# Kernel optimization log

Measured on AMD Instinct MI355X. Metric: run time of the kernel, lower is better.

The kernel has to match this reference:

```python
import jax, jax.numpy as jnp
import numpy as np

N_NODES = 100000
N_EDGES = 3200000


def gcn_conv(x, edge_index, W, b, num_nodes):
    # PyG GCNConv: linear transform, add self-loops, symmetric degree norm, scatter-add, bias
    h = x @ W  # [N, out]
    src = jnp.concatenate([edge_index[0], jnp.arange(num_nodes)])  # self-loops
    dst = jnp.concatenate([edge_index[1], jnp.arange(num_nodes)])
    deg = jax.ops.segment_sum(jnp.ones_like(dst, dtype=h.dtype), dst, num_segments=num_nodes)
    dinv = jnp.where(deg > 0, jax.lax.rsqrt(deg), 0.0)
    norm = dinv[src] * dinv[dst]  # [E+N]
    msg = h[src] * norm[:, None]  # gather + scale
    out = jax.ops.segment_sum(msg, dst, num_segments=num_nodes)  # scatter-add
    return out + b


def setup_inputs() -> dict:
    key = jax.random.key(0)
    k1, k2, k3, k4 = jax.random.split(key, 4)
    x = jax.random.normal(k1, (N_NODES, 18), dtype=jnp.float32)
    edge_index = jax.random.randint(k2, (2, N_EDGES), 0, N_NODES, dtype=jnp.int64)
    W1 = jax.random.normal(k3, (18, 64), dtype=jnp.float32) * (1.0 / np.sqrt(18))
    b1 = jnp.zeros((64,), dtype=jnp.float32)
    W2 = jax.random.normal(k4, (64, 32), dtype=jnp.float32) * (1.0 / np.sqrt(64))
    b2 = jnp.zeros((32,), dtype=jnp.float32)
    return {"x": x, "edge_index": edge_index, "W1": W1, "b1": b1, "W2": W2, "b2": b2}


def reference(x, edge_index, W1, b1, W2, b2):
    h = jax.nn.relu(gcn_conv(x, edge_index, W1, b1, N_NODES))
    return gcn_conv(h, edge_index, W2, b2, N_NODES)
```

## Files before the change

kernel.cpp:

```cpp
#include <hip/hip_runtime.h>
#include <hip/hip_fp16.h>

#define F0 18
#define F1 64
#define F2 32
#define BSHIFT 8
#define BNODES 256
#define CHUNK 8192
#define NSTRIPE 8
#define CAPS 1280
#define CAPB (CAPS * NSTRIPE)

__global__ __launch_bounds__(256) void scatter32_kernel(const int* __restrict__ ei,
                                                        int* __restrict__ bcur,
                                                        unsigned int* __restrict__ stage,
                                                        int E, int NB) {
    __shared__ int lh[512];
    __shared__ int lb[512];
    int t = threadIdx.x;
    int s = blockIdx.x & (NSTRIPE - 1);
    for (int i = t; i < NB; i += 256) lh[i] = 0;
    __syncthreads();
    int e0 = blockIdx.x * CHUNK, e1 = min(e0 + CHUNK, E);
    for (int e = e0 + t; e < e1; e += 256)
        atomicAdd(&lh[ei[E + e] >> BSHIFT], 1);
    __syncthreads();
    for (int i = t; i < NB; i += 256) {
        int c = lh[i];
        lb[i] = c ? atomicAdd(&bcur[i * NSTRIPE + s], c) : 0;
        lh[i] = 0;
    }
    __syncthreads();
    for (int e = e0 + t; e < e1; e += 256) {
        int sN = ei[e], d = ei[E + e];
        int b = d >> BSHIFT;
        int off = lb[b] + atomicAdd(&lh[b], 1);
        if (off < CAPS)
            stage[(size_t)(b * NSTRIPE + s) * CAPS + off] =
                ((unsigned)(d & 255) << 24) | (unsigned)sN;
    }
}

__global__ __launch_bounds__(1024) void bucketfill_kernel(const unsigned int* __restrict__ stage,
                                                          const int* __restrict__ bcur,
                                                          int* __restrict__ rps,
                                                          int* __restrict__ rpe,
                                                          float* __restrict__ dinv,
                                                          int* __restrict__ csr,
                                                          const float* __restrict__ x,
                                                          __half* __restrict__ xp, int n) {
    __shared__ unsigned int sbuf[CAPB];
    __shared__ int lcnt[BNODES];
    __shared__ int lofs[BNODES];
    __shared__ float ldv[BNODES];
    __shared__ int segofs[NSTRIPE + 1];
    int b = blockIdx.x;
    int base = b << BSHIFT;
    int nn = min(BNODES, n - base);
    int estart = b * CAPB;
    int t = threadIdx.x;

    if (t == 0) {
        int acc = 0;
        for (int s = 0; s < NSTRIPE; ++s) {
            segofs[s] = acc;
            acc += min(bcur[b * NSTRIPE + s], CAPS);
        }
        segofs[NSTRIPE] = acc;
    }
    if (t < BNODES) lcnt[t] = 0;
    __syncthreads();
    int ecnt = segofs[NSTRIPE];

    for (int s = 0; s < NSTRIPE; ++s) {
        int so = segofs[s], cs = segofs[s + 1] - so;
        const unsigned int* src = stage + (size_t)(b * NSTRIPE + s) * CAPS;
        for (int i = t; i < cs; i += 1024) sbuf[so + i] = src[i];
    }
    __syncthreads();

    for (int e = t; e < ecnt; e += 1024)
        atomicAdd(&lcnt[sbuf[e] >> 24], 1);
    __syncthreads();

    int v = 0;
    if (t < BNODES) { v = (t < nn) ? lcnt[t] : 0; lofs[t] = v; }
    __syncthreads();
    for (int off = 1; off < BNODES; off <<= 1) {
        int xv = 0;
        if (t < BNODES && t >= off) xv = lofs[t - off];
        __syncthreads();
        if (t < BNODES) lofs[t] += xv;
        __syncthreads();
    }
    if (t < nn) {
        float dv = rsqrtf((float)(v + 1));
        rps[base + t] = estart + lofs[t] - v;
        rpe[base + t] = estart + lofs[t];
        dinv[base + t] = dv;
        ldv[t] = dv;
    }
    __syncthreads();
    if (t < BNODES) lcnt[t] = lofs[t] - v;
    __syncthreads();

    for (int e = t; e < ecnt; e += 1024) {
        unsigned int pk = sbuf[e];
        int d = pk >> 24;
        int pos = atomicAdd(&lcnt[d], 1);
        csr[estart + pos] = (int)(pk & 0xffffffu);
    }
    for (int idx = t; idx < nn * 32; idx += 1024) {
        int lv = idx >> 5, j = idx & 31;
        float val = (j < F0) ? ldv[lv] * x[(size_t)(base + lv) * F0 + j] : 0.f;
        xp[(size_t)(base + lv) * 32 + j] = __float2half(val);
    }
}

struct __align__(8) h4v { __half2 a, b; };

__global__ __launch_bounds__(256) void agg32h_kernel(const __half* __restrict__ tab,
                                                     const int* __restrict__ csr,
                                                     const int* __restrict__ rps,
                                                     const int* __restrict__ rpe,
                                                     const float* __restrict__ dinv,
                                                     const float* __restrict__ bias,
                                                     float* __restrict__ outp, int n) {
    int wid = (blockIdx.x * 256 + threadIdx.x) >> 6;
    int lane = threadIdx.x & 63;
    if (wid >= n) return;
    int sub = lane >> 3;
    int q = (lane & 7) << 2;
    int beg = rps[wid], end = rpe[wid];
    float4 acc = make_float4(0.f, 0.f, 0.f, 0.f);
    if (sub == 0) {
        h4v sv = *(const h4v*)&tab[(size_t)wid * 32 + q];
        float2 f0 = __half22float2(sv.a), f1 = __half22float2(sv.b);
        acc.x = f0.x; acc.y = f0.y; acc.z = f1.x; acc.w = f1.y;
    }
    int e = beg + sub;
    for (; e + 8 < end; e += 16) {
        int s0 = csr[e], s1 = csr[e + 8];
        h4v v0 = *(const h4v*)&tab[(size_t)s0 * 32 + q];
        h4v v1 = *(const h4v*)&tab[(size_t)s1 * 32 + q];
        float2 a0 = __half22float2(v0.a), b0 = __half22float2(v0.b);
        float2 a1 = __half22float2(v1.a), b1 = __half22float2(v1.b);
        acc.x += a0.x + a1.x; acc.y += a0.y + a1.y;
        acc.z += b0.x + b1.x; acc.w += b0.y + b1.y;
    }
    for (; e < end; e += 8) {
        int s0 = csr[e];
        h4v v0 = *(const h4v*)&tab[(size_t)s0 * 32 + q];
        float2 a0 = __half22float2(v0.a), b0 = __half22float2(v0.b);
        acc.x += a0.x; acc.y += a0.y; acc.z += b0.x; acc.w += b0.y;
    }
    for (int off = 8; off < 64; off <<= 1) {
        acc.x += __shfl_xor(acc.x, off, 64);
        acc.y += __shfl_xor(acc.y, off, 64);
        acc.z += __shfl_xor(acc.z, off, 64);
        acc.w += __shfl_xor(acc.w, off, 64);
    }
    if (sub == 0) {
        float dv = dinv[wid];
        float4 r;
        r.x = acc.x * dv; r.y = acc.y * dv; r.z = acc.z * dv; r.w = acc.w * dv;
        if (bias) { r.x += bias[q]; r.y += bias[q + 1]; r.z += bias[q + 2]; r.w += bias[q + 3]; }
        *(float4*)&outp[(size_t)wid * 32 + q] = r;
    }
}

__global__ __launch_bounds__(256) void gemm_fused_kernel(const float* __restrict__ ax,
                                                         const float* __restrict__ W1,
                                                         const float* __restrict__ b1,
                                                         const float* __restrict__ W2,
                                                         const float* __restrict__ dinv,
                                                         __half* __restrict__ h2p, int n) {
    __shared__ float W1s[F0 * F1];
    __shared__ float W2s[F1 * F2];
    __shared__ float hid[8][F1];
    __shared__ float axs[8][32];
    int t = threadIdx.x;
    for (int i = t; i < F0 * F1; i += 256) W1s[i] = W1[i];
    for (int i = t; i < F1 * F2; i += 256) W2s[i] = W2[i];
    int lv = t >> 5, j = t & 31;
    int v = blockIdx.x * 8 + lv;
    if (v < n) axs[lv][j] = ax[(size_t)v * 32 + j];
    __syncthreads();
    float h0 = b1[j], h1 = b1[j + 32];
#pragma unroll
    for (int k = 0; k < F0; ++k) {
        float a = axs[lv][k];
        h0 += a * W1s[k * F1 + j];
        h1 += a * W1s[k * F1 + j + 32];
    }
    hid[lv][j] = fmaxf(h0, 0.f);
    hid[lv][j + 32] = fmaxf(h1, 0.f);
    __syncthreads();
    float acc = 0.f;
#pragma unroll
    for (int k = 0; k < F1; ++k) acc += hid[lv][k] * W2s[k * F2 + j];
    if (v < n) h2p[(size_t)v * 32 + j] = __float2half(acc * dinv[v]);
}


extern "C" void kernel_launch(void* const* d_in, const int* in_sizes, int n_in,
                              void* d_out, int out_size, void* d_ws, size_t ws_size,
                              hipStream_t stream) {
    const float* x  = (const float*)d_in[0];
    const int*   ei = (const int*)d_in[1];
    const float* W1 = (const float*)d_in[2];
    const float* b1 = (const float*)d_in[3];
    const float* W2 = (const float*)d_in[4];
    const float* b2 = (const float*)d_in[5];
    float* out = (float*)d_out;

    int n = in_sizes[0] / F0;
    int E = in_sizes[1] / 2;
    int NB = (n + BNODES - 1) >> BSHIFT;

    char* ws = (char*)d_ws;
    size_t o = 0;
    auto alloc = [&](size_t bytes) {
        char* p = ws + o;
        o = (o + bytes + 255) & ~(size_t)255;
        return p;
    };
    int*   rps   = (int*)alloc((size_t)n * 4);
    int*   rpe   = (int*)alloc((size_t)n * 4);
    float* dinv  = (float*)alloc((size_t)n * 4);
    int*   bcur  = (int*)alloc((size_t)NB * NSTRIPE * 4);
    int*   csr   = (int*)alloc((size_t)NB * CAPB * 4);
    unsigned int* stage = (unsigned int*)alloc((size_t)NB * CAPB * 4);
    float* ax    = (float*)alloc((size_t)n * 32 * 4);
    __half* xp   = (__half*)alloc((size_t)n * 32 * 2);
    __half* h2p  = (__half*)stage;
    (void)ws_size; (void)n_in; (void)out_size;

    int nchunks = (E + CHUNK - 1) / CHUNK;

    hipMemsetAsync(bcur, 0, (size_t)NB * NSTRIPE * 4, stream);
    scatter32_kernel<<<nchunks, 256, 0, stream>>>(ei, bcur, stage, E, NB);
    bucketfill_kernel<<<NB, 1024, 0, stream>>>(stage, bcur, rps, rpe, dinv, csr, x, xp, n);

    agg32h_kernel<<<(n + 3) / 4, 256, 0, stream>>>(xp, csr, rps, rpe, dinv, nullptr, ax, n);
    gemm_fused_kernel<<<(n + 7) / 8, 256, 0, stream>>>(ax, W1, b1, W2, dinv, h2p, n);
    agg32h_kernel<<<(n + 3) / 4, 256, 0, stream>>>(h2p, csr, rps, rpe, dinv, b2, out, n);
}
```

Baseline: 217.0 us.

## Split gathered feature tables into narrow 16-column and 2-column half tables

The padded 32-wide half feature table is replaced by column-split tables. For layer 1 that is a 16-column table plus a 2-column table, so the 14 padding columns are no longer gathered. Layer 2 becomes two 16-column halves aggregated in separate passes, which keeps each gathered row at 32 bytes so it fits the cache better. Index loads are marked nontemporal. In exchange there are more kernel launches and the CSR index array is read more times, and the bias pointer arithmetic has to be correct for the split halves.

```diff
diff --git a/kernel.cpp b/kernel.cpp
--- a/kernel.cpp
+++ b/kernel.cpp
@@ -23,7 +23,7 @@
     __syncthreads();
     int e0 = blockIdx.x * CHUNK, e1 = min(e0 + CHUNK, E);
     for (int e = e0 + t; e < e1; e += 256)
-        atomicAdd(&lh[ei[E + e] >> BSHIFT], 1);
+        atomicAdd(&lh[__builtin_nontemporal_load(&ei[E + e]) >> BSHIFT], 1);
     __syncthreads();
     for (int i = t; i < NB; i += 256) {
         int c = lh[i];
@@ -32,7 +32,8 @@
     }
     __syncthreads();
     for (int e = e0 + t; e < e1; e += 256) {
-        int sN = ei[e], d = ei[E + e];
+        int sN = __builtin_nontemporal_load(&ei[e]);
+        int d  = __builtin_nontemporal_load(&ei[E + e]);
         int b = d >> BSHIFT;
         int off = lb[b] + atomicAdd(&lh[b], 1);
         if (off < CAPS)
@@ -48,7 +49,9 @@
                                                           float* __restrict__ dinv,
                                                           int* __restrict__ csr,
                                                           const float* __restrict__ x,
-                                                          __half* __restrict__ xp, int n) {
+                                                          __half* __restrict__ xpA,
+                                                          __half* __restrict__ xpB,
+                                                          int n) {
     __shared__ unsigned int sbuf[CAPB];
     __shared__ int lcnt[BNODES];
     __shared__ int lofs[BNODES];
@@ -110,51 +113,58 @@
         int pos = atomicAdd(&lcnt[d], 1);
         csr[estart + pos] = (int)(pk & 0xffffffu);
     }
-    for (int idx = t; idx < nn * 32; idx += 1024) {
-        int lv = idx >> 5, j = idx & 31;
-        float val = (j < F0) ? ldv[lv] * x[(size_t)(base + lv) * F0 + j] : 0.f;
-        xp[(size_t)(base + lv) * 32 + j] = __float2half(val);
+    for (int idx = t; idx < nn * 16; idx += 1024) {
+        int lv = idx >> 4, j = idx & 15;
+        xpA[(size_t)(base + lv) * 16 + j] =
+            __float2half(ldv[lv] * x[(size_t)(base + lv) * F0 + j]);
+    }
+    for (int idx = t; idx < nn * 2; idx += 1024) {
+        int lv = idx >> 1, j = idx & 1;
+        xpB[(size_t)(base + lv) * 2 + j] =
+            __float2half(ldv[lv] * x[(size_t)(base + lv) * F0 + 16 + j]);
     }
 }
 
 struct __align__(8) h4v { __half2 a, b; };
 
-__global__ __launch_bounds__(256) void agg32h_kernel(const __half* __restrict__ tab,
+__global__ __launch_bounds__(256) void agg16h_kernel(const __half* __restrict__ tab,
                                                      const int* __restrict__ csr,
                                                      const int* __restrict__ rps,
                                                      const int* __restrict__ rpe,
                                                      const float* __restrict__ dinv,
                                                      const float* __restrict__ bias,
-                                                     float* __restrict__ outp, int n) {
+                                                     float* __restrict__ outp,
+                                                     int colofs, int n) {
     int wid = (blockIdx.x * 256 + threadIdx.x) >> 6;
     int lane = threadIdx.x & 63;
     if (wid >= n) return;
-    int sub = lane >> 3;
-    int q = (lane & 7) << 2;
+    int sub = lane >> 2;
+    int q = (lane & 3) << 2;
     int beg = rps[wid], end = rpe[wid];
     float4 acc = make_float4(0.f, 0.f, 0.f, 0.f);
     if (sub == 0) {
-        h4v sv = *(const h4v*)&tab[(size_t)wid * 32 + q];
+        h4v sv = *(const h4v*)&tab[(size_t)wid * 16 + q];
         float2 f0 = __half22float2(sv.a), f1 = __half22float2(sv.b);
         acc.x = f0.x; acc.y = f0.y; acc.z = f1.x; acc.w = f1.y;
     }
     int e = beg + sub;
-    for (; e + 8 < end; e += 16) {
-        int s0 = csr[e], s1 = csr[e + 8];
-        h4v v0 = *(const h4v*)&tab[(size_t)s0 * 32 + q];
-        h4v v1 = *(const h4v*)&tab[(size_t)s1 * 32 + q];
+    for (; e + 16 < end; e += 32) {
+        int s0 = __builtin_nontemporal_load(&csr[e]);
+        int s1 = __builtin_nontemporal_load(&csr[e + 16]);
+        h4v v0 = *(const h4v*)&tab[(size_t)s0 * 16 + q];
+        h4v v1 = *(const h4v*)&tab[(size_t)s1 * 16 + q];
         float2 a0 = __half22float2(v0.a), b0 = __half22float2(v0.b);
         float2 a1 = __half22float2(v1.a), b1 = __half22float2(v1.b);
         acc.x += a0.x + a1.x; acc.y += a0.y + a1.y;
         acc.z += b0.x + b1.x; acc.w += b0.y + b1.y;
     }
-    for (; e < end; e += 8) {
-        int s0 = csr[e];
-        h4v v0 = *(const h4v*)&tab[(size_t)s0 * 32 + q];
+    for (; e < end; e += 16) {
+        int s0 = __builtin_nontemporal_load(&csr[e]);
+        h4v v0 = *(const h4v*)&tab[(size_t)s0 * 16 + q];
         float2 a0 = __half22float2(v0.a), b0 = __half22float2(v0.b);
         acc.x += a0.x; acc.y += a0.y; acc.z += b0.x; acc.w += b0.y;
     }
-    for (int off = 8; off < 64; off <<= 1) {
+    for (int off = 4; off < 64; off <<= 1) {
         acc.x += __shfl_xor(acc.x, off, 64);
         acc.y += __shfl_xor(acc.y, off, 64);
         acc.z += __shfl_xor(acc.z, off, 64);
@@ -165,7 +175,35 @@
         float4 r;
         r.x = acc.x * dv; r.y = acc.y * dv; r.z = acc.z * dv; r.w = acc.w * dv;
         if (bias) { r.x += bias[q]; r.y += bias[q + 1]; r.z += bias[q + 2]; r.w += bias[q + 3]; }
-        *(float4*)&outp[(size_t)wid * 32 + q] = r;
+        *(float4*)&outp[(size_t)wid * 32 + colofs + q] = r;
+    }
+}
+
+__global__ __launch_bounds__(256) void agg2h_kernel(const __half* __restrict__ tab2,
+                                                    const int* __restrict__ csr,
+                                                    const int* __restrict__ rps,
+                                                    const int* __restrict__ rpe,
+                                                    const float* __restrict__ dinv,
+                                                    float* __restrict__ outp, int n) {
+    int wid = (blockIdx.x * 256 + threadIdx.x) >> 6;
+    int lane = threadIdx.x & 63;
+    if (wid >= n) return;
+    int beg = rps[wid], end = rpe[wid];
+    float ax = 0.f, ay = 0.f;
+    for (int e = beg + lane; e < end; e += 64) {
+        int s = __builtin_nontemporal_load(&csr[e]);
+        float2 f = __half22float2(*(const __half2*)&tab2[(size_t)s * 2]);
+        ax += f.x; ay += f.y;
+    }
+    for (int off = 1; off < 64; off <<= 1) {
+        ax += __shfl_xor(ax, off, 64);
+        ay += __shfl_xor(ay, off, 64);
+    }
+    if (lane == 0) {
+        float2 f = __half22float2(*(const __half2*)&tab2[(size_t)wid * 2]);
+        float dv = dinv[wid];
+        outp[(size_t)wid * 32 + 16] = (ax + f.x) * dv;
+        outp[(size_t)wid * 32 + 17] = (ay + f.y) * dv;
     }
 }
 
@@ -174,7 +212,9 @@
                                                          const float* __restrict__ b1,
                                                          const float* __restrict__ W2,
                                                          const float* __restrict__ dinv,
-                                                         __half* __restrict__ h2p, int n) {
+                                                         __half* __restrict__ h2A,
+                                                         __half* __restrict__ h2B,
+                                                         int n) {
     __shared__ float W1s[F0 * F1];
     __shared__ float W2s[F1 * F2];
     __shared__ float hid[8][F1];
@@ -199,7 +239,11 @@
     float acc = 0.f;
 #pragma unroll
     for (int k = 0; k < F1; ++k) acc += hid[lv][k] * W2s[k * F2 + j];
-    if (v < n) h2p[(size_t)v * 32 + j] = __float2half(acc * dinv[v]);
+    if (v < n) {
+        float r = acc * dinv[v];
+        if (j < 16) h2A[(size_t)v * 16 + j] = __float2half(r);
+        else        h2B[(size_t)v * 16 + (j - 16)] = __float2half(r);
+    }
 }
 
 
@@ -232,17 +276,21 @@
     int*   csr   = (int*)alloc((size_t)NB * CAPB * 4);
     unsigned int* stage = (unsigned int*)alloc((size_t)NB * CAPB * 4);
     float* ax    = (float*)alloc((size_t)n * 32 * 4);
-    __half* xp   = (__half*)alloc((size_t)n * 32 * 2);
-    __half* h2p  = (__half*)stage;
+    __half* xpA  = (__half*)alloc((size_t)n * 16 * 2);
+    __half* xpB  = (__half*)alloc((size_t)n * 2 * 2);
+    __half* h2A  = (__half*)stage;
+    __half* h2B  = (__half*)(stage + (size_t)n * 16);
     (void)ws_size; (void)n_in; (void)out_size;
 
     int nchunks = (E + CHUNK - 1) / CHUNK;
 
     hipMemsetAsync(bcur, 0, (size_t)NB * NSTRIPE * 4, stream);
     scatter32_kernel<<<nchunks, 256, 0, stream>>>(ei, bcur, stage, E, NB);
-    bucketfill_kernel<<<NB, 1024, 0, stream>>>(stage, bcur, rps, rpe, dinv, csr, x, xp, n);
-
-    agg32h_kernel<<<(n + 3) / 4, 256, 0, stream>>>(xp, csr, rps, rpe, dinv, nullptr, ax, n);
-    gemm_fused_kernel<<<(n + 7) / 8, 256, 0, stream>>>(ax, W1, b1, W2, dinv, h2p, n);
-    agg32h_kernel<<<(n + 3) / 4, 256, 0, stream>>>(h2p, csr, rps, rpe, dinv, b2, out, n);
-}
+    bucketfill_kernel<<<NB, 1024, 0, stream>>>(stage, bcur, rps, rpe, dinv, csr, x, xpA, xpB, n);
+
+    agg16h_kernel<<<(n + 3) / 4, 256, 0, stream>>>(xpA, csr, rps, rpe, dinv, nullptr, ax, 0, n);
+    agg2h_kernel<<<(n + 3) / 4, 256, 0, stream>>>(xpB, csr, rps, rpe, dinv, ax, n);
+    gemm_fused_kernel<<<(n + 7) / 8, 256, 0, stream>>>(ax, W1, b1, W2, dinv, h2A, h2B, n);
+    agg16h_kernel<<<(n + 3) / 4, 256, 0, stream>>>(h2A, csr, rps, rpe, dinv, b2, out, 0, n);
+    agg16h_kernel<<<(n + 3) / 4, 256, 0, stream>>>(h2B, csr, rps, rpe, dinv, b2 + 16, out, 16, n);
+}
```

Measured after the change: 294.6 us. +35.8%, slower.

## Split aggregation into two source-range phases for gather cache locality

Applied to the files above, without the earlier changes.

Each CSR row is partitioned by whether the source index falls in the lower or upper half of the nodes, and each aggregation runs as two passes, each gathering only from one half of the feature table. The goal is to shrink the gather working set per pass so it fits better in cache. The cost is an extra fp32 partial buffer written and re-read, two more launches, and a 512-bin scan in bucketfill. The scatter kernel also moves to 1024 threads with nontemporal edge loads.

```diff
diff --git a/kernel.cpp b/kernel.cpp
--- a/kernel.cpp
+++ b/kernel.cpp
@@ -11,28 +11,29 @@
 #define CAPS 1280
 #define CAPB (CAPS * NSTRIPE)
 
-__global__ __launch_bounds__(256) void scatter32_kernel(const int* __restrict__ ei,
-                                                        int* __restrict__ bcur,
-                                                        unsigned int* __restrict__ stage,
-                                                        int E, int NB) {
+__global__ __launch_bounds__(1024) void scatter32_kernel(const int* __restrict__ ei,
+                                                         int* __restrict__ bcur,
+                                                         unsigned int* __restrict__ stage,
+                                                         int E, int NB) {
     __shared__ int lh[512];
     __shared__ int lb[512];
     int t = threadIdx.x;
     int s = blockIdx.x & (NSTRIPE - 1);
-    for (int i = t; i < NB; i += 256) lh[i] = 0;
+    if (t < 512) lh[t] = 0;
     __syncthreads();
     int e0 = blockIdx.x * CHUNK, e1 = min(e0 + CHUNK, E);
-    for (int e = e0 + t; e < e1; e += 256)
-        atomicAdd(&lh[ei[E + e] >> BSHIFT], 1);
-    __syncthreads();
-    for (int i = t; i < NB; i += 256) {
+    for (int e = e0 + t; e < e1; e += 1024)
+        atomicAdd(&lh[__builtin_nontemporal_load(&ei[E + e]) >> BSHIFT], 1);
+    __syncthreads();
+    for (int i = t; i < NB; i += 1024) {
         int c = lh[i];
         lb[i] = c ? atomicAdd(&bcur[i * NSTRIPE + s], c) : 0;
         lh[i] = 0;
     }
     __syncthreads();
-    for (int e = e0 + t; e < e1; e += 256) {
-        int sN = ei[e], d = ei[E + e];
+    for (int e = e0 + t; e < e1; e += 1024) {
+        int sN = __builtin_nontemporal_load(&ei[e]);
+        int d  = __builtin_nontemporal_load(&ei[E + e]);
         int b = d >> BSHIFT;
         int off = lb[b] + atomicAdd(&lh[b], 1);
         if (off < CAPS)
@@ -44,14 +45,16 @@
 __global__ __launch_bounds__(1024) void bucketfill_kernel(const unsigned int* __restrict__ stage,
                                                           const int* __restrict__ bcur,
                                                           int* __restrict__ rps,
+                                                          int* __restrict__ mid,
                                                           int* __restrict__ rpe,
                                                           float* __restrict__ dinv,
                                                           int* __restrict__ csr,
                                                           const float* __restrict__ x,
-                                                          __half* __restrict__ xp, int n) {
+                                                          __half* __restrict__ xp,
+                                                          int halfN, int n) {
     __shared__ unsigned int sbuf[CAPB];
-    __shared__ int lcnt[BNODES];
-    __shared__ int lofs[BNODES];
+    __shared__ int lcnt2[512];
+    __shared__ int lofs2[512];
     __shared__ float ldv[BNODES];
     __shared__ int segofs[NSTRIPE + 1];
     int b = blockIdx.x;
@@ -68,7 +71,7 @@
         }
         segofs[NSTRIPE] = acc;
     }
-    if (t < BNODES) lcnt[t] = 0;
+    if (t < 512) lcnt2[t] = 0;
     __syncthreads();
     int ecnt = segofs[NSTRIPE];
 
@@ -79,36 +82,46 @@
     }
     __syncthreads();
 
-    for (int e = t; e < ecnt; e += 1024)
-        atomicAdd(&lcnt[sbuf[e] >> 24], 1);
-    __syncthreads();
-
-    int v = 0;
-    if (t < BNODES) { v = (t < nn) ? lcnt[t] : 0; lofs[t] = v; }
-    __syncthreads();
-    for (int off = 1; off < BNODES; off <<= 1) {
+    for (int e = t; e < ecnt; e += 1024) {
+        unsigned int pk = sbuf[e];
+        int idx = (int)((pk >> 24) << 1) | ((int)(pk & 0xffffffu) >= halfN ? 1 : 0);
+        atomicAdd(&lcnt2[idx], 1);
+    }
+    __syncthreads();
+
+    if (t < 512) lofs2[t] = lcnt2[t];
+    __syncthreads();
+    for (int off = 1; off < 512; off <<= 1) {
         int xv = 0;
-        if (t < BNODES && t >= off) xv = lofs[t - off];
+        if (t < 512 && t >= off) xv = lofs2[t - off];
         __syncthreads();
-        if (t < BNODES) lofs[t] += xv;
+        if (t < 512) lofs2[t] += xv;
         __syncthreads();
     }
     if (t < nn) {
-        float dv = rsqrtf((float)(v + 1));
-        rps[base + t] = estart + lofs[t] - v;
-        rpe[base + t] = estart + lofs[t];
+        int cA = lcnt2[2 * t], cB = lcnt2[2 * t + 1];
+        int incl = lofs2[2 * t + 1];
+        int eB = incl - cB, eA = eB - cA;
+        float dv = rsqrtf((float)(cA + cB + 1));
+        rps[base + t] = estart + eA;
+        mid[base + t] = estart + eB;
+        rpe[base + t] = estart + incl;
         dinv[base + t] = dv;
         ldv[t] = dv;
     }
     __syncthreads();
-    if (t < BNODES) lcnt[t] = lofs[t] - v;
+    int cur = 0;
+    if (t < 512) cur = lofs2[t] - lcnt2[t];
+    __syncthreads();
+    if (t < 512) lcnt2[t] = cur;
     __syncthreads();
 
     for (int e = t; e < ecnt; e += 1024) {
         unsigned int pk = sbuf[e];
-        int d = pk >> 24;
-        int pos = atomicAdd(&lcnt[d], 1);
-        csr[estart + pos] = (int)(pk & 0xffffffu);
+        int src = (int)(pk & 0xffffffu);
+        int idx = (int)((pk >> 24) << 1) | (src >= halfN ? 1 : 0);
+        int pos = atomicAdd(&lcnt2[idx], 1);
+        csr[estart + pos] = src;
     }
     for (int idx = t; idx < nn * 32; idx += 1024) {
         int lv = idx >> 5, j = idx & 31;
@@ -119,21 +132,24 @@
 
 struct __align__(8) h4v { __half2 a, b; };
 
-__global__ __launch_bounds__(256) void agg32h_kernel(const __half* __restrict__ tab,
-                                                     const int* __restrict__ csr,
-                                                     const int* __restrict__ rps,
-                                                     const int* __restrict__ rpe,
-                                                     const float* __restrict__ dinv,
-                                                     const float* __restrict__ bias,
-                                                     float* __restrict__ outp, int n) {
+__global__ __launch_bounds__(256) void aggph_kernel(const __half* __restrict__ tab,
+                                                    const int* __restrict__ csr,
+                                                    const int* __restrict__ begA,
+                                                    const int* __restrict__ endA,
+                                                    const float* __restrict__ dinv,
+                                                    const float* __restrict__ bias,
+                                                    const float* __restrict__ part,
+                                                    float* __restrict__ outp,
+                                                    int phase, int halfN, int n) {
     int wid = (blockIdx.x * 256 + threadIdx.x) >> 6;
     int lane = threadIdx.x & 63;
     if (wid >= n) return;
     int sub = lane >> 3;
     int q = (lane & 7) << 2;
-    int beg = rps[wid], end = rpe[wid];
+    int beg = begA[wid], end = endA[wid];
     float4 acc = make_float4(0.f, 0.f, 0.f, 0.f);
-    if (sub == 0) {
+    bool selfHere = (phase == 0) ? (wid < halfN) : (wid >= halfN);
+    if (sub == 0 && selfHere) {
         h4v sv = *(const h4v*)&tab[(size_t)wid * 32 + q];
         float2 f0 = __half22float2(sv.a), f1 = __half22float2(sv.b);
         acc.x = f0.x; acc.y = f0.y; acc.z = f1.x; acc.w = f1.y;
@@ -161,10 +177,16 @@
         acc.w += __shfl_xor(acc.w, off, 64);
     }
     if (sub == 0) {
-        float dv = dinv[wid];
         float4 r;
-        r.x = acc.x * dv; r.y = acc.y * dv; r.z = acc.z * dv; r.w = acc.w * dv;
-        if (bias) { r.x += bias[q]; r.y += bias[q + 1]; r.z += bias[q + 2]; r.w += bias[q + 3]; }
+        if (phase == 0) {
+            r = acc;
+        } else {
+            const float4 p = *(const float4*)&part[(size_t)wid * 32 + q];
+            float dv = dinv[wid];
+            r.x = (acc.x + p.x) * dv; r.y = (acc.y + p.y) * dv;
+            r.z = (acc.z + p.z) * dv; r.w = (acc.w + p.w) * dv;
+            if (bias) { r.x += bias[q]; r.y += bias[q + 1]; r.z += bias[q + 2]; r.w += bias[q + 3]; }
+        }
         *(float4*)&outp[(size_t)wid * 32 + q] = r;
     }
 }
@@ -217,6 +239,7 @@
     int n = in_sizes[0] / F0;
     int E = in_sizes[1] / 2;
     int NB = (n + BNODES - 1) >> BSHIFT;
+    int halfN = n / 2;
 
     char* ws = (char*)d_ws;
     size_t o = 0;
@@ -226,6 +249,7 @@
         return p;
     };
     int*   rps   = (int*)alloc((size_t)n * 4);
+    int*   midp  = (int*)alloc((size_t)n * 4);
     int*   rpe   = (int*)alloc((size_t)n * 4);
     float* dinv  = (float*)alloc((size_t)n * 4);
     int*   bcur  = (int*)alloc((size_t)NB * NSTRIPE * 4);
@@ -233,16 +257,20 @@
     unsigned int* stage = (unsigned int*)alloc((size_t)NB * CAPB * 4);
     float* ax    = (float*)alloc((size_t)n * 32 * 4);
     __half* xp   = (__half*)alloc((size_t)n * 32 * 2);
-    __half* h2p  = (__half*)stage;
+    __half* h2p  = (__half*)alloc((size_t)n * 32 * 2);
+    float* part  = (float*)stage;
     (void)ws_size; (void)n_in; (void)out_size;
 
     int nchunks = (E + CHUNK - 1) / CHUNK;
 
     hipMemsetAsync(bcur, 0, (size_t)NB * NSTRIPE * 4, stream);
-    scatter32_kernel<<<nchunks, 256, 0, stream>>>(ei, bcur, stage, E, NB);
-    bucketfill_kernel<<<NB, 1024, 0, stream>>>(stage, bcur, rps, rpe, dinv, csr, x, xp, n);
-
-    agg32h_kernel<<<(n + 3) / 4, 256, 0, stream>>>(xp, csr, rps, rpe, dinv, nullptr, ax, n);
+    scatter32_kernel<<<nchunks, 1024, 0, stream>>>(ei, bcur, stage, E, NB);
+    bucketfill_kernel<<<NB, 1024, 0, stream>>>(stage, bcur, rps, midp, rpe, dinv, csr, x, xp, halfN, n);
+
+    int aggblocks = (n + 3) / 4;
+    aggph_kernel<<<aggblocks, 256, 0, stream>>>(xp, csr, rps, midp, dinv, nullptr, nullptr, part, 0, halfN, n);
+    aggph_kernel<<<aggblocks, 256, 0, stream>>>(xp, csr, midp, rpe, dinv, nullptr, part, ax, 1, halfN, n);
     gemm_fused_kernel<<<(n + 7) / 8, 256, 0, stream>>>(ax, W1, b1, W2, dinv, h2p, n);
-    agg32h_kernel<<<(n + 3) / 4, 256, 0, stream>>>(h2p, csr, rps, rpe, dinv, b2, out, n);
-}
+    aggph_kernel<<<aggblocks, 256, 0, stream>>>(h2p, csr, rps, midp, dinv, nullptr, nullptr, part, 0, halfN, n);
+    aggph_kernel<<<aggblocks, 256, 0, stream>>>(h2p, csr, midp, rpe, dinv, b2, part, out, 1, halfN, n);
+}
```

Result: slower. 257.5 us (+18.7%).

## Fuse first-layer aggregation with MLP and widen scatter blocks

Applied to the files above, without the earlier changes.

Merges the first neighbour aggregation with the dense W1/ReLU/W2 transform in one kernel. Each wavefront aggregates one node, stages the result in LDS and runs both matrix products in place, so the fp32 intermediate buffer and its global write and read disappear, along with one launch. The scatter kernel moves to 1024-thread blocks with nontemporal loads of the edge list. The trade-off is that every 4-node block now reloads 16KB of weights into LDS, which adds L2 traffic and LDS pressure.

```diff
diff --git a/kernel.cpp b/kernel.cpp
--- a/kernel.cpp
+++ b/kernel.cpp
@@ -11,28 +11,29 @@
 #define CAPS 1280
 #define CAPB (CAPS * NSTRIPE)
 
-__global__ __launch_bounds__(256) void scatter32_kernel(const int* __restrict__ ei,
-                                                        int* __restrict__ bcur,
-                                                        unsigned int* __restrict__ stage,
-                                                        int E, int NB) {
+__global__ __launch_bounds__(1024) void scatter32_kernel(const int* __restrict__ ei,
+                                                         int* __restrict__ bcur,
+                                                         unsigned int* __restrict__ stage,
+                                                         int E, int NB) {
     __shared__ int lh[512];
     __shared__ int lb[512];
     int t = threadIdx.x;
     int s = blockIdx.x & (NSTRIPE - 1);
-    for (int i = t; i < NB; i += 256) lh[i] = 0;
+    if (t < 512) lh[t] = 0;
     __syncthreads();
     int e0 = blockIdx.x * CHUNK, e1 = min(e0 + CHUNK, E);
-    for (int e = e0 + t; e < e1; e += 256)
-        atomicAdd(&lh[ei[E + e] >> BSHIFT], 1);
-    __syncthreads();
-    for (int i = t; i < NB; i += 256) {
+    for (int e = e0 + t; e < e1; e += 1024)
+        atomicAdd(&lh[__builtin_nontemporal_load(&ei[E + e]) >> BSHIFT], 1);
+    __syncthreads();
+    for (int i = t; i < NB; i += 1024) {
         int c = lh[i];
         lb[i] = c ? atomicAdd(&bcur[i * NSTRIPE + s], c) : 0;
         lh[i] = 0;
     }
     __syncthreads();
-    for (int e = e0 + t; e < e1; e += 256) {
-        int sN = ei[e], d = ei[E + e];
+    for (int e = e0 + t; e < e1; e += 1024) {
+        int sN = __builtin_nontemporal_load(&ei[e]);
+        int d  = __builtin_nontemporal_load(&ei[E + e]);
         int b = d >> BSHIFT;
         int off = lb[b] + atomicAdd(&lh[b], 1);
         if (off < CAPS)
@@ -119,6 +120,82 @@
 
 struct __align__(8) h4v { __half2 a, b; };
 
+__global__ __launch_bounds__(256) void agg1_mlp_kernel(const __half* __restrict__ tab,
+                                                       const int* __restrict__ csr,
+                                                       const int* __restrict__ rps,
+                                                       const int* __restrict__ rpe,
+                                                       const float* __restrict__ dinv,
+                                                       const float* __restrict__ W1,
+                                                       const float* __restrict__ b1,
+                                                       const float* __restrict__ W2,
+                                                       __half* __restrict__ h2p, int n) {
+    __shared__ float W1s[32 * F1];
+    __shared__ float W2s[F1 * F2];
+    __shared__ float ax_lds[4][32];
+    __shared__ float hid_lds[4][F1];
+    int t = threadIdx.x;
+    for (int i = t; i < 32 * F1; i += 256) {
+        int k = i >> 6;
+        W1s[i] = (k < F0) ? W1[(size_t)k * F1 + (i & 63)] : 0.f;
+    }
+    for (int i = t; i < F1 * F2; i += 256) W2s[i] = W2[i];
+    __syncthreads();
+
+    int wid = (blockIdx.x * 256 + t) >> 6;
+    int lane = t & 63;
+    int slot = (t >> 6) & 3;
+    if (wid >= n) return;
+    int sub = lane >> 3;
+    int q = (lane & 7) << 2;
+    int beg = rps[wid], end = rpe[wid];
+    float4 acc = make_float4(0.f, 0.f, 0.f, 0.f);
+    if (sub == 0) {
+        h4v sv = *(const h4v*)&tab[(size_t)wid * 32 + q];
+        float2 f0 = __half22float2(sv.a), f1 = __half22float2(sv.b);
+        acc.x = f0.x; acc.y = f0.y; acc.z = f1.x; acc.w = f1.y;
+    }
+    int e = beg + sub;
+    for (; e + 8 < end; e += 16) {
+        int s0 = csr[e], s1 = csr[e + 8];
+        h4v v0 = *(const h4v*)&tab[(size_t)s0 * 32 + q];
+        h4v v1 = *(const h4v*)&tab[(size_t)s1 * 32 + q];
+        float2 a0 = __half22float2(v0.a), b0 = __half22float2(v0.b);
+        float2 a1 = __half22float2(v1.a), b1_ = __half22float2(v1.b);
+        acc.x += a0.x + a1.x; acc.y += a0.y + a1.y;
+        acc.z += b0.x + b1_.x; acc.w += b0.y + b1_.y;
+    }
+    for (; e < end; e += 8) {
+        int s0 = csr[e];
+        h4v v0 = *(const h4v*)&tab[(size_t)s0 * 32 + q];
+        float2 a0 = __half22float2(v0.a), b0 = __half22float2(v0.b);
+        acc.x += a0.x; acc.y += a0.y; acc.z += b0.x; acc.w += b0.y;
+    }
+    for (int off = 8; off < 64; off <<= 1) {
+        acc.x += __shfl_xor(acc.x, off, 64);
+        acc.y += __shfl_xor(acc.y, off, 64);
+        acc.z += __shfl_xor(acc.z, off, 64);
+        acc.w += __shfl_xor(acc.w, off, 64);
+    }
+    float dv = dinv[wid];
+    if (sub == 0) {
+        ax_lds[slot][q + 0] = acc.x * dv;
+        ax_lds[slot][q + 1] = acc.y * dv;
+        ax_lds[slot][q + 2] = acc.z * dv;
+        ax_lds[slot][q + 3] = acc.w * dv;
+    }
+    float h = b1[lane];
+#pragma unroll
+    for (int k = 0; k < 32; ++k) h += ax_lds[slot][k] * W1s[k * F1 + lane];
+    hid_lds[slot][lane] = fmaxf(h, 0.f);
+    int j = lane & 31;
+    int k0 = (lane >> 5) * 32;
+    float p = 0.f;
+#pragma unroll
+    for (int kk = 0; kk < 32; ++kk) p += hid_lds[slot][k0 + kk] * W2s[(k0 + kk) * F2 + j];
+    p += __shfl_xor(p, 32, 64);
+    if (lane < 32) h2p[(size_t)wid * 32 + j] = __float2half(p * dv);
+}
+
 __global__ __launch_bounds__(256) void agg32h_kernel(const __half* __restrict__ tab,
                                                      const int* __restrict__ csr,
                                                      const int* __restrict__ rps,
@@ -163,43 +240,12 @@
     if (sub == 0) {
         float dv = dinv[wid];
         float4 r;
-        r.x = acc.x * dv; r.y = acc.y * dv; r.z = acc.z * dv; r.w = acc.w * dv;
-        if (bias) { r.x += bias[q]; r.y += bias[q + 1]; r.z += bias[q + 2]; r.w += bias[q + 3]; }
+        r.x = acc.x * dv + bias[q];
+        r.y = acc.y * dv + bias[q + 1];
+        r.z = acc.z * dv + bias[q + 2];
+        r.w = acc.w * dv + bias[q + 3];
         *(float4*)&outp[(size_t)wid * 32 + q] = r;
     }
-}
-
-__global__ __launch_bounds__(256) void gemm_fused_kernel(const float* __restrict__ ax,
-                                                         const float* __restrict__ W1,
-                                                         const float* __restrict__ b1,
-                                                         const float* __restrict__ W2,
-                                                         const float* __restrict__ dinv,
-                                                         __half* __restrict__ h2p, int n) {
-    __shared__ float W1s[F0 * F1];
-    __shared__ float W2s[F1 * F2];
-    __shared__ float hid[8][F1];
-    __shared__ float axs[8][32];
-    int t = threadIdx.x;
-    for (int i = t; i < F0 * F1; i += 256) W1s[i] = W1[i];
-    for (int i = t; i < F1 * F2; i += 256) W2s[i] = W2[i];
-    int lv = t >> 5, j = t & 31;
-    int v = blockIdx.x * 8 + lv;
-    if (v < n) axs[lv][j] = ax[(size_t)v * 32 + j];
-    __syncthreads();
-    float h0 = b1[j], h1 = b1[j + 32];
-#pragma unroll
-    for (int k = 0; k < F0; ++k) {
-        float a = axs[lv][k];
-        h0 += a * W1s[k * F1 + j];
-        h1 += a * W1s[k * F1 + j + 32];
-    }
-    hid[lv][j] = fmaxf(h0, 0.f);
-    hid[lv][j + 32] = fmaxf(h1, 0.f);
-    __syncthreads();
-    float acc = 0.f;
-#pragma unroll
-    for (int k = 0; k < F1; ++k) acc += hid[lv][k] * W2s[k * F2 + j];
-    if (v < n) h2p[(size_t)v * 32 + j] = __float2half(acc * dinv[v]);
 }
 
 
@@ -231,7 +277,6 @@
     int*   bcur  = (int*)alloc((size_t)NB * NSTRIPE * 4);
     int*   csr   = (int*)alloc((size_t)NB * CAPB * 4);
     unsigned int* stage = (unsigned int*)alloc((size_t)NB * CAPB * 4);
-    float* ax    = (float*)alloc((size_t)n * 32 * 4);
     __half* xp   = (__half*)alloc((size_t)n * 32 * 2);
     __half* h2p  = (__half*)stage;
     (void)ws_size; (void)n_in; (void)out_size;
@@ -239,10 +284,10 @@
     int nchunks = (E + CHUNK - 1) / CHUNK;
 
     hipMemsetAsync(bcur, 0, (size_t)NB * NSTRIPE * 4, stream);
-    scatter32_kernel<<<nchunks, 256, 0, stream>>>(ei, bcur, stage, E, NB);
+    scatter32_kernel<<<nchunks, 1024, 0, stream>>>(ei, bcur, stage, E, NB);
     bucketfill_kernel<<<NB, 1024, 0, stream>>>(stage, bcur, rps, rpe, dinv, csr, x, xp, n);
 
-    agg32h_kernel<<<(n + 3) / 4, 256, 0, stream>>>(xp, csr, rps, rpe, dinv, nullptr, ax, n);
-    gemm_fused_kernel<<<(n + 7) / 8, 256, 0, stream>>>(ax, W1, b1, W2, dinv, h2p, n);
-    agg32h_kernel<<<(n + 3) / 4, 256, 0, stream>>>(h2p, csr, rps, rpe, dinv, b2, out, n);
-}
+    int aggblocks = (n + 3) / 4;
+    agg1_mlp_kernel<<<aggblocks, 256, 0, stream>>>(xp, csr, rps, rpe, dinv, W1, b1, W2, h2p, n);
+    agg32h_kernel<<<aggblocks, 256, 0, stream>>>(h2p, csr, rps, rpe, dinv, b2, out, n);
+}
```

Result: slower. 237.0 us (+9.3%).
